# Optimization experiments

Hardware: AMD Instinct MI355X
Metric: run time of the kernel (lower is better)

## Reference

```python
import jax, jax.numpy as jnp
import numpy as np

TEMP1, TEMP2, TEMP3 = 4.0, 5.0, 10.0  # forward() default temps
EPS = 1e-8


def setup_inputs() -> dict:
    key = jax.random.key(0)
    k1, k2 = jax.random.split(key)
    B, L, D = 64, 64, 512
    return {
        "ecg_embs": jax.random.normal(k1, (B, L, D), dtype=jnp.float32),
        "sent_embs": jax.random.normal(k2, (B, L, D), dtype=jnp.float32),
    }


def reference(ecg_embs, sent_embs):
    # Fully-batched version of the original per-sample Python loop.
    # i indexes the sentence (query) sample, j the ecg (context) sample.
    B, L, D = ecg_embs.shape
    # scores[i,j,s,q] = <ecg[j,s,:], sent[i,q,:]>  == contextT @ query in torch
    scores = jnp.einsum('jsd,iqd->ijsq', ecg_embs, sent_embs)
    # 1st softmax over query axis q
    attn = jax.nn.softmax(scores, axis=-1)
    # transpose to (i,j,q,s), temperature-scale, 2nd softmax over source axis s
    attn = jax.nn.softmax(TEMP1 * jnp.swapaxes(attn, -1, -2), axis=-1)  # (i,j,q,s)
    # weightedContext[i,j,q,:] = sum_s attn[i,j,q,s] * ecg[j,s,:]
    wctx = jnp.einsum('ijqs,jsd->ijqd', attn, ecg_embs)
    sent = sent_embs[:, None]  # (i,1,q,d) broadcast over j
    w12 = jnp.sum(sent * wctx, axis=-1)
    w1 = jnp.linalg.norm(sent, axis=-1)
    w2 = jnp.linalg.norm(wctx, axis=-1)
    cos = w12 / jnp.maximum(w1 * w2, EPS)  # (i,j,q)
    # row_sim.mul_(temp2).exp_().sum(dim=1).log() ; similarities[j,i] (cat along dim=1)
    sim = TEMP3 * jnp.log(jnp.sum(jnp.exp(TEMP2 * cos), axis=-1)).T  # (j,i)
    labels = jnp.arange(B)
    logp0 = jax.nn.log_softmax(sim, axis=-1)
    logp1 = jax.nn.log_softmax(sim.T, axis=-1)
    loss0 = -jnp.mean(logp0[labels, labels])
    loss1 = -jnp.mean(logp1[labels, labels])
    # att_maps: list of attn[i] from iteration i == diagonal (i==j) attention,
    # each shaped (1, queryL, ih=1, iw=sourceL); stacked -> (B, 1, L, 1, L)
    att_maps = attn[labels, labels][:, None, :, None, :]
    return (loss0 + loss1) / 2.0, att_maps
```

## Files before the change

### kernel.cpp

```cpp
#include <hip/hip_runtime.h>
#include <math.h>

typedef __attribute__((ext_vector_type(8))) short short8;
typedef __attribute__((ext_vector_type(4))) float f32x4;
typedef unsigned int uint;
typedef unsigned short ushort;

#define T1 4.0f
#define T2 5.0f
#define T3 10.0f
#define EPSF 1e-8f
#define SST 68

__device__ inline ushort f2bf(float x) {
    union { float f; uint u; } a; a.f = x;
    uint r = a.u + 0x7FFFu + ((a.u >> 16) & 1u);
    return (ushort)(r >> 16);
}
__device__ inline float bf2f(ushort h) {
    union { uint u; float f; } a; a.u = ((uint)h) << 16;
    return a.f;
}

#define GLDS(gsrc, ldst) \
    __builtin_amdgcn_global_load_lds( \
        (const __attribute__((address_space(1))) uint*)(gsrc), \
        (__attribute__((address_space(3))) uint*)(ldst), 16, 0, 0)

__global__ __launch_bounds__(256) void prep_kernel(
        const float* __restrict__ ecg, const float* __restrict__ sent,
        char* __restrict__ EH, char* __restrict__ EL,
        char* __restrict__ SH, char* __restrict__ SL,
        char* __restrict__ Gp, float* __restrict__ w1, uint* __restrict__ donecnt) {
    __shared__ float partial[256];
    const int bid = blockIdx.x;
    const int tensor = bid >> 6, idx = bid & 63;
    if (bid == 0 && threadIdx.x == 0) *donecnt = 0;
    const float* src = (tensor ? sent : ecg) + (size_t)idx * 32768;
    char* dh = (tensor ? SH : EH) + (size_t)idx * 65536;
    char* dl = (tensor ? SL : EL) + (size_t)idx * 65536;
    const int tid = threadIdx.x;
    const int r = tid & 63;
    float s2 = 0.f;
    #pragma unroll
    for (int it = 0; it < 4; it++) {
        int kc = it * 4 + (tid >> 6);
        const float* p = src + r * 512 + kc * 32;
        char* oh = dh + kc * 4096 + r * 64;
        char* ol = dl + kc * 4096 + r * 64;
        #pragma unroll
        for (int c = 0; c < 4; c++) {
            float4 v0 = *(const float4*)(p + c * 8);
            float4 v1 = *(const float4*)(p + c * 8 + 4);
            float x[8] = {v0.x, v0.y, v0.z, v0.w, v1.x, v1.y, v1.z, v1.w};
            uint hw[4], lw[4];
            #pragma unroll
            for (int e = 0; e < 4; e++) {
                float a0 = x[2 * e], a1 = x[2 * e + 1];
                ushort h0 = f2bf(a0), h1 = f2bf(a1);
                hw[e] = (uint)h0 | ((uint)h1 << 16);
                ushort l0 = f2bf(a0 - bf2f(h0)), l1 = f2bf(a1 - bf2f(h1));
                lw[e] = (uint)l0 | ((uint)l1 << 16);
                s2 += a0 * a0 + a1 * a1;
            }
            int phys = (c + (r >> 1)) & 3;
            uint4 H; H.x = hw[0]; H.y = hw[1]; H.z = hw[2]; H.w = hw[3];
            *(uint4*)(oh + phys * 16) = H;
            uint4 L; L.x = lw[0]; L.y = lw[1]; L.z = lw[2]; L.w = lw[3];
            *(uint4*)(ol + phys * 16) = L;
        }
    }
    partial[tid] = s2;
    __syncthreads();
    if (tensor == 1) {
        if (tid < 64) {
            float t = partial[tid] + partial[tid + 64] + partial[tid + 128] + partial[tid + 192];
            w1[idx * 64 + tid] = sqrtf(t);
        }
        return;
    }

    {
        const char* srcH = EH + (size_t)idx * 65536;
        const char* srcL = EL + (size_t)idx * 65536;
        const int wv = tid >> 6, lane = tid & 63;
        const int wq = wv >> 1, wn = wv & 1;
        const int quad = lane >> 4, ln = lane & 15;

        int ao[2], bo[2];
        #pragma unroll
        for (int mi = 0; mi < 2; mi++) {
            int R = 32 * wq + 16 * mi + ln;
            ao[mi] = R * 64 + ((quad + (R >> 1)) & 3) * 16;
        }
        #pragma unroll
        for (int ni = 0; ni < 2; ni++) {
            int R = 32 * wn + 16 * ni + ln;
            bo[ni] = R * 64 + ((quad + (R >> 1)) & 3) * 16;
        }

        f32x4 acc[2][2];
        #pragma unroll
        for (int a = 0; a < 2; a++)
            #pragma unroll
            for (int b = 0; b < 2; b++) acc[a][b] = (f32x4){0.f, 0.f, 0.f, 0.f};

        #pragma unroll 2
        for (int kc = 0; kc < 16; kc++) {
            const char* ph = srcH + (size_t)kc * 4096;
            const char* pl = srcL + (size_t)kc * 4096;
            short8 ah[2], al[2], bh[2], bl[2];
            #pragma unroll
            for (int mi = 0; mi < 2; mi++) {
                ah[mi] = *(const short8*)(ph + ao[mi]);
                al[mi] = *(const short8*)(pl + ao[mi]);
            }
            #pragma unroll
            for (int ni = 0; ni < 2; ni++) {
                bh[ni] = *(const short8*)(ph + bo[ni]);
                bl[ni] = *(const short8*)(pl + bo[ni]);
            }
            #pragma unroll
            for (int mi = 0; mi < 2; mi++)
                #pragma unroll
                for (int ni = 0; ni < 2; ni++) {
                    acc[mi][ni] = __builtin_amdgcn_mfma_f32_16x16x32_bf16(ah[mi], bh[ni], acc[mi][ni], 0, 0, 0);
                    acc[mi][ni] = __builtin_amdgcn_mfma_f32_16x16x32_bf16(ah[mi], bl[ni], acc[mi][ni], 0, 0, 0);
                    acc[mi][ni] = __builtin_amdgcn_mfma_f32_16x16x32_bf16(al[mi], bh[ni], acc[mi][ni], 0, 0, 0);
                }
        }
        #pragma unroll
        for (int mi = 0; mi < 2; mi++)
            #pragma unroll
            for (int ni = 0; ni < 2; ni++)
                #pragma unroll
                for (int rr = 0; rr < 4; rr++) {
                    int t = 32 * wq + 16 * mi + quad * 4 + rr;
                    int u = 32 * wn + 16 * ni + ln;
                    float g = acc[mi][ni][rr];
                    ushort h = f2bf(g);
                    ushort l = f2bf(g - bf2f(h));
                    char* base = Gp + (size_t)idx * 16384 + t * 128 + (((u >> 3) + t) & 7) * 16 + (u & 7) * 2;
                    *(ushort*)base = h;
                    *(ushort*)(base + 8192) = l;
                }
    }
}

__global__ __launch_bounds__(256, 4) void pair_kernel(
        const char* __restrict__ EH, const char* __restrict__ EL,
        const char* __restrict__ SH, const char* __restrict__ SL,
        const char* __restrict__ Gp, const float* __restrict__ w1g,
        float* __restrict__ simval, float* __restrict__ out, uint* __restrict__ donecnt) {

    __shared__ __align__(16) char lds[33792];
    __shared__ __align__(16) float mz[64];
    __shared__ float w12all[256], w2all[256];
    __shared__ uint lastflag;

    const int tid = threadIdx.x;
    const int bn = blockIdx.x;
    const int xcd = bn & 7, slot = bn >> 3;
    const int T = xcd * 8 + (slot >> 4);
    const int wp = slot & 15;
    const int bi = (T >> 3) * 4 + (wp >> 2);
    const int bj = (T & 7) * 4 + (wp & 3);
    const int i0 = bi * 2, j0 = bj * 2;

    const int wv = tid >> 6, lane = tid & 63;
    const int wq = wv >> 1, wn = wv & 1;
    const int quad = lane >> 4, ln = lane & 15;

    int aoff[4], boff[4];
    #pragma unroll
    for (int mi = 0; mi < 4; mi++) {
        int R = 64 * (mi >> 1) + 32 * wq + 16 * (mi & 1) + ln;
        aoff[mi] = R * 64 + ((quad + (R >> 1)) & 3) * 16;
    }
    #pragma unroll
    for (int ni = 0; ni < 4; ni++) {
        int R = 64 * (ni >> 1) + 32 * wn + 16 * (ni & 1) + ln;
        boff[ni] = 16384 + R * 64 + ((quad + (R >> 1)) & 3) * 16;
    }

    const char* gA; const char* gB; int ldoff;
    if (wv == 0)      { gA = EH + (size_t)j0 * 65536;       gB = EH + (size_t)(j0 + 1) * 65536; ldoff = 0; }
    else if (wv == 1) { gA = EL + (size_t)j0 * 65536;       gB = EL + (size_t)(j0 + 1) * 65536; ldoff = 8192; }
    else if (wv == 2) { gA = SH + (size_t)i0 * 65536;       gB = SH + (size_t)(i0 + 1) * 65536; ldoff = 16384; }
    else              { gA = SL + (size_t)i0 * 65536;       gB = SL + (size_t)(i0 + 1) * 65536; ldoff = 24576; }
    gA += lane * 16; gB += lane * 16;

    f32x4 acc[4][4];
    #pragma unroll
    for (int a = 0; a < 4; a++)
        #pragma unroll
        for (int b = 0; b < 4; b++) acc[a][b] = (f32x4){0.f, 0.f, 0.f, 0.f};

    for (int kc = 0; kc < 16; kc++) {
        #pragma unroll
        for (int n = 0; n < 4; n++) GLDS(gA + n * 1024, lds + ldoff + n * 1024);
        #pragma unroll
        for (int n = 0; n < 4; n++) GLDS(gB + n * 1024, lds + ldoff + 4096 + n * 1024);
        gA += 4096; gB += 4096;
        __syncthreads();
        short8 bh[4], bl[4];
        #pragma unroll
        for (int ni = 0; ni < 4; ni++) {
            bh[ni] = *(const short8*)(lds + boff[ni]);
            bl[ni] = *(const short8*)(lds + boff[ni] + 8192);
        }
        #pragma unroll
        for (int mi = 0; mi < 4; mi++) {
            short8 ah = *(const short8*)(lds + aoff[mi]);
            short8 al = *(const short8*)(lds + aoff[mi] + 8192);
            #pragma unroll
            for (int ni = 0; ni < 4; ni++) {
                acc[mi][ni] = __builtin_amdgcn_mfma_f32_16x16x32_bf16(ah, bh[ni], acc[mi][ni], 0, 0, 0);
                acc[mi][ni] = __builtin_amdgcn_mfma_f32_16x16x32_bf16(ah, bl[ni], acc[mi][ni], 0, 0, 0);
                acc[mi][ni] = __builtin_amdgcn_mfma_f32_16x16x32_bf16(al, bh[ni], acc[mi][ni], 0, 0, 0);
            }
        }
        __syncthreads();
    }

    float* SsT = (float*)lds;
    float* yQ  = (float*)lds;
    char*  Pb  = lds + 17408;

    #pragma unroll
    for (int pr = 0; pr < 4; pr++) {
        const int a = pr >> 1, b = pr & 1;
        const int i = i0 + b, j = j0 + a;

        #pragma unroll
        for (int dm = 0; dm < 2; dm++)
            #pragma unroll
            for (int dn = 0; dn < 2; dn++) {
                int s0 = 32 * wq + 16 * dm + quad * 4;
                int q  = 32 * wn + 16 * dn + ln;
                *(f32x4*)(SsT + q * SST + s0) = acc[2 * a + dm][2 * b + dn];
            }
        __syncthreads();

        {
            const int s = tid >> 2, c = tid & 3;
            float vv[16]; float m = -1e30f;
            #pragma unroll
            for (int t = 0; t < 16; t++) {
                int tt = (t + 4 * c) & 15;
                vv[t] = SsT[(16 * c + tt) * SST + s];
                m = fmaxf(m, vv[t]);
            }
            m = fmaxf(m, __shfl_xor(m, 1));
            m = fmaxf(m, __shfl_xor(m, 2));
            float sum = 0.f;
            #pragma unroll
            for (int t = 0; t < 16; t++) sum += __expf(vv[t] - m);
            sum += __shfl_xor(sum, 1);
            sum += __shfl_xor(sum, 2);
            if (c == 0) mz[s] = m + __logf(sum);
        }
        __syncthreads();

        {
            const int q = tid >> 2, c = tid & 3;
            float sc[16], at[16];
            #pragma unroll
            for (int r4 = 0; r4 < 4; r4++)
                *(f32x4*)(sc + 4 * r4) = *(const f32x4*)(SsT + q * SST + 16 * c + 4 * r4);
            float mzv[16];
            #pragma unroll
            for (int r4 = 0; r4 < 4; r4++)
                *(f32x4*)(mzv + 4 * r4) = *(const f32x4*)(mz + 16 * c + 4 * r4);
            float m2 = -1e30f;
            #pragma unroll
            for (int t = 0; t < 16; t++) {
                at[t] = __expf(sc[t] - mzv[t]);
                m2 = fmaxf(m2, T1 * at[t]);
            }
            m2 = fmaxf(m2, __shfl_xor(m2, 1));
            m2 = fmaxf(m2, __shfl_xor(m2, 2));
            float sum = 0.f;
            #pragma unroll
            for (int t = 0; t < 16; t++) { at[t] = __expf(T1 * at[t] - m2); sum += at[t]; }
            sum += __shfl_xor(sum, 1);
            sum += __shfl_xor(sum, 2);
            float inv = 1.f / sum;
            float p12 = 0.f;
            #pragma unroll
            for (int t = 0; t < 16; t++) { at[t] *= inv; p12 += at[t] * sc[t]; }
            p12 += __shfl_xor(p12, 1);
            p12 += __shfl_xor(p12, 2);
            if (c == 0) w12all[pr * 64 + q] = p12;

            if (i == j) {
                float* om = out + 1 + (size_t)i * 4096;
                #pragma unroll
                for (int t = 0; t < 16; t++) om[q * 64 + c * 16 + t] = at[t];
            }

            uint hw[8], lw[8];
            #pragma unroll
            for (int e = 0; e < 8; e++) {
                ushort h0 = f2bf(at[2 * e]), h1 = f2bf(at[2 * e + 1]);
                hw[e] = (uint)h0 | ((uint)h1 << 16);
                ushort l0 = f2bf(at[2 * e] - bf2f(h0)), l1 = f2bf(at[2 * e + 1] - bf2f(h1));
                lw[e] = (uint)l0 | ((uint)l1 << 16);
            }
            int p0 = (2 * c + q) & 7, p1 = (2 * c + 1 + q) & 7;
            uint4 W;
            W.x = hw[0]; W.y = hw[1]; W.z = hw[2]; W.w = hw[3];
            *(uint4*)(Pb + q * 128 + p0 * 16) = W;
            W.x = hw[4]; W.y = hw[5]; W.z = hw[6]; W.w = hw[7];
            *(uint4*)(Pb + q * 128 + p1 * 16) = W;
            W.x = lw[0]; W.y = lw[1]; W.z = lw[2]; W.w = lw[3];
            *(uint4*)(Pb + 8192 + q * 128 + p0 * 16) = W;
            W.x = lw[4]; W.y = lw[5]; W.z = lw[6]; W.w = lw[7];
            *(uint4*)(Pb + 8192 + q * 128 + p1 * 16) = W;
        }
        __syncthreads();

        {
            const char* gs = Gp + (size_t)j * 16384 + wv * 4096 + lane * 16;
            char* gd = lds + wv * 4096;
            GLDS(gs,        gd);
            GLDS(gs + 1024, gd + 1024);
            GLDS(gs + 2048, gd + 2048);
            GLDS(gs + 3072, gd + 3072);
        }
        __syncthreads();

        f32x4 acc2[2][2];
        #pragma unroll
        for (int x = 0; x < 2; x++)
            #pragma unroll
            for (int y = 0; y < 2; y++) acc2[x][y] = (f32x4){0.f, 0.f, 0.f, 0.f};
        #pragma unroll
        for (int ch = 0; ch < 2; ch++) {
            short8 pah[2], pal[2], gbh[2], gbl[2];
            #pragma unroll
            for (int m2i = 0; m2i < 2; m2i++) {
                int q = 32 * wq + 16 * m2i + ln;
                int ph = ((ch * 4 + quad) + q) & 7;
                pah[m2i] = *(const short8*)(Pb + q * 128 + ph * 16);
                pal[m2i] = *(const short8*)(Pb + 8192 + q * 128 + ph * 16);
            }
            #pragma unroll
            for (int n2i = 0; n2i < 2; n2i++) {
                int u = 32 * wn + 16 * n2i + ln;
                int ph = ((ch * 4 + quad) + u) & 7;
                gbh[n2i] = *(const short8*)(lds + u * 128 + ph * 16);
                gbl[n2i] = *(const short8*)(lds + 8192 + u * 128 + ph * 16);
            }
            #pragma unroll
            for (int m2i = 0; m2i < 2; m2i++)
                #pragma unroll
                for (int n2i = 0; n2i < 2; n2i++) {
                    acc2[m2i][n2i] = __builtin_amdgcn_mfma_f32_16x16x32_bf16(pah[m2i], gbh[n2i], acc2[m2i][n2i], 0, 0, 0);
                    acc2[m2i][n2i] = __builtin_amdgcn_mfma_f32_16x16x32_bf16(pah[m2i], gbl[n2i], acc2[m2i][n2i], 0, 0, 0);
                    acc2[m2i][n2i] = __builtin_amdgcn_mfma_f32_16x16x32_bf16(pal[m2i], gbh[n2i], acc2[m2i][n2i], 0, 0, 0);
                }
        }
        __syncthreads();

        #pragma unroll
        for (int m2i = 0; m2i < 2; m2i++)
            #pragma unroll
            for (int n2i = 0; n2i < 2; n2i++) {
                int t  = 32 * wn + 16 * n2i + ln;
                int qb = 32 * wq + 16 * m2i + quad * 4;
                yQ[(qb + 0) * SST + t] = acc2[m2i][n2i][0];
                yQ[(qb + 1) * SST + t] = acc2[m2i][n2i][1];
                yQ[(qb + 2) * SST + t] = acc2[m2i][n2i][2];
                yQ[(qb + 3) * SST + t] = acc2[m2i][n2i][3];
            }
        __syncthreads();

        {
            const int q = tid >> 2, c = tid & 3;
            int p0 = (2 * c + q) & 7, p1 = (2 * c + 1 + q) & 7;
            uint4 H0 = *(const uint4*)(Pb + q * 128 + p0 * 16);
            uint4 H1 = *(const uint4*)(Pb + q * 128 + p1 * 16);
            uint4 L0 = *(const uint4*)(Pb + 8192 + q * 128 + p0 * 16);
            uint4 L1 = *(const uint4*)(Pb + 8192 + q * 128 + p1 * 16);
            uint hw[8] = {H0.x,H0.y,H0.z,H0.w, H1.x,H1.y,H1.z,H1.w};
            uint lw[8] = {L0.x,L0.y,L0.z,L0.w, L1.x,L1.y,L1.z,L1.w};
            float vy[16];
            #pragma unroll
            for (int r4 = 0; r4 < 4; r4++)
                *(f32x4*)(vy + 4 * r4) = *(const f32x4*)(yQ + q * SST + 16 * c + 4 * r4);
            float s = 0.f;
            #pragma unroll
            for (int e = 0; e < 8; e++) {
                float q0v = bf2f((ushort)(hw[e] & 0xFFFFu)) + bf2f((ushort)(lw[e] & 0xFFFFu));
                float q1v = bf2f((ushort)(hw[e] >> 16))     + bf2f((ushort)(lw[e] >> 16));
                s += q0v * vy[2 * e];
                s += q1v * vy[2 * e + 1];
            }
            s += __shfl_xor(s, 1);
            s += __shfl_xor(s, 2);
            if (c == 0) w2all[pr * 64 + q] = s;
        }
        __syncthreads();
    }

    {
        const int pr = wv;
        const int ii = i0 + (pr & 1), jj = j0 + (pr >> 1);
        float w2 = sqrtf(fmaxf(w2all[pr * 64 + lane], 0.f));
        float cosv = w12all[pr * 64 + lane] / fmaxf(w1g[ii * 64 + lane] * w2, EPSF);
        float e = __expf(T2 * cosv);
        #pragma unroll
        for (int off = 32; off; off >>= 1) e += __shfl_down(e, off);
        if (lane == 0) simval[ii * 64 + jj] = T3 * __logf(e);
    }
    __syncthreads();

    if (tid == 0) {
        __threadfence();
        uint prev = atomicAdd(donecnt, 1u);
        lastflag = (prev == 1023u);
    }
    __syncthreads();
    if (lastflag) {
        __threadfence();
        float* v = (float*)lds;
        #pragma unroll
        for (int k = 0; k < 4; k++)
            ((float4*)v)[tid + k * 256] = ((const float4*)simval)[tid + k * 256];
        __syncthreads();
        if (tid < 64) {
            int i = tid;
            float rmax = -1e30f, cmax = -1e30f;
            for (int jj = 0; jj < 64; jj++) {
                rmax = fmaxf(rmax, v[i * 64 + jj]);
                cmax = fmaxf(cmax, v[jj * 64 + i]);
            }
            float rs = 0.f, cs = 0.f;
            for (int jj = 0; jj < 64; jj++) {
                rs += __expf(v[i * 64 + jj] - rmax);
                cs += __expf(v[jj * 64 + i] - cmax);
            }
            float rlse = rmax + __logf(rs);
            float clse = cmax + __logf(cs);
            float part = 2.f * v[i * 64 + i] - rlse - clse;
            #pragma unroll
            for (int off = 32; off; off >>= 1) part += __shfl_down(part, off);
            if (i == 0) out[0] = -part / 128.f;
        }
    }
}

extern "C" void kernel_launch(void* const* d_in, const int* in_sizes, int n_in,
                              void* d_out, int out_size, void* d_ws, size_t ws_size,
                              hipStream_t stream) {
    (void)in_sizes; (void)n_in; (void)out_size; (void)ws_size;
    const float* ecg  = (const float*)d_in[0];
    const float* sent = (const float*)d_in[1];
    float* out = (float*)d_out;

    char* ws = (char*)d_ws;
    float* w1v  = (float*)ws;
    float* simv = (float*)(ws + 16384);
    uint*  dcnt = (uint*)(ws + 32768);
    char* EH = ws + 33024;
    char* EL = EH + (size_t)64 * 65536;
    char* SH = EL + (size_t)64 * 65536;
    char* SL = SH + (size_t)64 * 65536;
    char* Gp = SL + (size_t)64 * 65536;

    prep_kernel <<<128, 256, 0, stream>>>(ecg, sent, EH, EL, SH, SL, Gp, w1v, dcnt);
    pair_kernel <<<1024, 256, 0, stream>>>(EH, EL, SH, SL, Gp, w1v, simv, out, dcnt);
}
```

Measured before the change: 165.2 us.

## Move final loss to separate kernel and store transposed y tile

Replaces the last-block atomic counter and threadfence scheme at the end of pair_kernel with a separate single-block loss kernel launched afterwards. The y tile (acc2) is now written to LDS transposed with one vectorized f32x4 store per fragment instead of four scalar stores. The w2 dot product then reads it with strided scalar LDS loads in place of the vectorized row loads. This drops the per-block atomic and fence work, but adds an extra kernel launch and may cause more LDS bank conflicts on the read side.

```diff
diff --git a/kernel.cpp b/kernel.cpp
--- a/kernel.cpp
+++ b/kernel.cpp
@@ -31,11 +31,10 @@
         const float* __restrict__ ecg, const float* __restrict__ sent,
         char* __restrict__ EH, char* __restrict__ EL,
         char* __restrict__ SH, char* __restrict__ SL,
-        char* __restrict__ Gp, float* __restrict__ w1, uint* __restrict__ donecnt) {
+        char* __restrict__ Gp, float* __restrict__ w1) {
     __shared__ float partial[256];
     const int bid = blockIdx.x;
     const int tensor = bid >> 6, idx = bid & 63;
-    if (bid == 0 && threadIdx.x == 0) *donecnt = 0;
     const float* src = (tensor ? sent : ecg) + (size_t)idx * 32768;
     char* dh = (tensor ? SH : EH) + (size_t)idx * 65536;
     char* dl = (tensor ? SL : EL) + (size_t)idx * 65536;
@@ -151,12 +150,11 @@
         const char* __restrict__ EH, const char* __restrict__ EL,
         const char* __restrict__ SH, const char* __restrict__ SL,
         const char* __restrict__ Gp, const float* __restrict__ w1g,
-        float* __restrict__ simval, float* __restrict__ out, uint* __restrict__ donecnt) {
+        float* __restrict__ simval, float* __restrict__ out) {
 
     __shared__ __align__(16) char lds[33792];
     __shared__ __align__(16) float mz[64];
     __shared__ float w12all[256], w2all[256];
-    __shared__ uint lastflag;
 
     const int tid = threadIdx.x;
     const int bn = blockIdx.x;
@@ -224,7 +222,7 @@
     }
 
     float* SsT = (float*)lds;
-    float* yQ  = (float*)lds;
+    float* yT  = (float*)lds;
     char*  Pb  = lds + 17408;
 
     #pragma unroll
@@ -367,12 +365,9 @@
         for (int m2i = 0; m2i < 2; m2i++)
             #pragma unroll
             for (int n2i = 0; n2i < 2; n2i++) {
+                int q0 = 32 * wq + 16 * m2i + quad * 4;
                 int t  = 32 * wn + 16 * n2i + ln;
-                int qb = 32 * wq + 16 * m2i + quad * 4;
-                yQ[(qb + 0) * SST + t] = acc2[m2i][n2i][0];
-                yQ[(qb + 1) * SST + t] = acc2[m2i][n2i][1];
-                yQ[(qb + 2) * SST + t] = acc2[m2i][n2i][2];
-                yQ[(qb + 3) * SST + t] = acc2[m2i][n2i][3];
+                *(f32x4*)(yT + t * SST + q0) = acc2[m2i][n2i];
             }
         __syncthreads();
 
@@ -385,17 +380,13 @@
             uint4 L1 = *(const uint4*)(Pb + 8192 + q * 128 + p1 * 16);
             uint hw[8] = {H0.x,H0.y,H0.z,H0.w, H1.x,H1.y,H1.z,H1.w};
             uint lw[8] = {L0.x,L0.y,L0.z,L0.w, L1.x,L1.y,L1.z,L1.w};
-            float vy[16];
-            #pragma unroll
-            for (int r4 = 0; r4 < 4; r4++)
-                *(f32x4*)(vy + 4 * r4) = *(const f32x4*)(yQ + q * SST + 16 * c + 4 * r4);
             float s = 0.f;
             #pragma unroll
             for (int e = 0; e < 8; e++) {
                 float q0v = bf2f((ushort)(hw[e] & 0xFFFFu)) + bf2f((ushort)(lw[e] & 0xFFFFu));
                 float q1v = bf2f((ushort)(hw[e] >> 16))     + bf2f((ushort)(lw[e] >> 16));
-                s += q0v * vy[2 * e];
-                s += q1v * vy[2 * e + 1];
+                s += q0v * yT[(16 * c + 2 * e) * SST + q];
+                s += q1v * yT[(16 * c + 2 * e + 1) * SST + q];
             }
             s += __shfl_xor(s, 1);
             s += __shfl_xor(s, 2);
@@ -414,40 +405,34 @@
         for (int off = 32; off; off >>= 1) e += __shfl_down(e, off);
         if (lane == 0) simval[ii * 64 + jj] = T3 * __logf(e);
     }
+}
+
+__global__ __launch_bounds__(256) void loss_kernel(const float* __restrict__ val,
+                                                   float* __restrict__ out) {
+    __shared__ float v[4096];
+    const int tid = threadIdx.x;
+    #pragma unroll
+    for (int k = 0; k < 4; k++)
+        ((float4*)v)[tid + k * 256] = ((const float4*)val)[tid + k * 256];
     __syncthreads();
-
-    if (tid == 0) {
-        __threadfence();
-        uint prev = atomicAdd(donecnt, 1u);
-        lastflag = (prev == 1023u);
-    }
-    __syncthreads();
-    if (lastflag) {
-        __threadfence();
-        float* v = (float*)lds;
-        #pragma unroll
-        for (int k = 0; k < 4; k++)
-            ((float4*)v)[tid + k * 256] = ((const float4*)simval)[tid + k * 256];
-        __syncthreads();
-        if (tid < 64) {
-            int i = tid;
-            float rmax = -1e30f, cmax = -1e30f;
-            for (int jj = 0; jj < 64; jj++) {
-                rmax = fmaxf(rmax, v[i * 64 + jj]);
-                cmax = fmaxf(cmax, v[jj * 64 + i]);
-            }
-            float rs = 0.f, cs = 0.f;
-            for (int jj = 0; jj < 64; jj++) {
-                rs += __expf(v[i * 64 + jj] - rmax);
-                cs += __expf(v[jj * 64 + i] - cmax);
-            }
-            float rlse = rmax + __logf(rs);
-            float clse = cmax + __logf(cs);
-            float part = 2.f * v[i * 64 + i] - rlse - clse;
-            #pragma unroll
-            for (int off = 32; off; off >>= 1) part += __shfl_down(part, off);
-            if (i == 0) out[0] = -part / 128.f;
-        }
+    if (tid < 64) {
+        int i = tid;
+        float rmax = -1e30f, cmax = -1e30f;
+        for (int jj = 0; jj < 64; jj++) {
+            rmax = fmaxf(rmax, v[i * 64 + jj]);
+            cmax = fmaxf(cmax, v[jj * 64 + i]);
+        }
+        float rs = 0.f, cs = 0.f;
+        for (int jj = 0; jj < 64; jj++) {
+            rs += __expf(v[i * 64 + jj] - rmax);
+            cs += __expf(v[jj * 64 + i] - cmax);
+        }
+        float rlse = rmax + __logf(rs);
+        float clse = cmax + __logf(cs);
+        float part = 2.f * v[i * 64 + i] - rlse - clse;
+        #pragma unroll
+        for (int off = 32; off; off >>= 1) part += __shfl_down(part, off);
+        if (i == 0) out[0] = -part / 128.f;
     }
 }
 
@@ -462,13 +447,13 @@
     char* ws = (char*)d_ws;
     float* w1v  = (float*)ws;
     float* simv = (float*)(ws + 16384);
-    uint*  dcnt = (uint*)(ws + 32768);
-    char* EH = ws + 33024;
+    char* EH = ws + 32768;
     char* EL = EH + (size_t)64 * 65536;
     char* SH = EL + (size_t)64 * 65536;
     char* SL = SH + (size_t)64 * 65536;
     char* Gp = SL + (size_t)64 * 65536;
 
-    prep_kernel <<<128, 256, 0, stream>>>(ecg, sent, EH, EL, SH, SL, Gp, w1v, dcnt);
-    pair_kernel <<<1024, 256, 0, stream>>>(EH, EL, SH, SL, Gp, w1v, simv, out, dcnt);
-}
+    prep_kernel <<<128, 256, 0, stream>>>(ecg, sent, EH, EL, SH, SL, Gp, w1v);
+    pair_kernel <<<1024, 256, 0, stream>>>(EH, EL, SH, SL, Gp, w1v, simv, out);
+    loss_kernel <<<1,   256, 0, stream>>>(simv, out);
+}
```

Result: faster. 158.7 us (-3.9%).
